# Optimization experiments

Measured on AMD Instinct MI355X. Metric: run time of the kernel, lower is better.

Reference implementation:

```python
import jax, jax.numpy as jnp
import numpy as np
from jax import lax

B, CIN, H, W = 32, 1, 128, 128
SC, CC = 128, 128          # simple / complex channels
C = SC + CC                # 256
KS, STRIDE, PAD = 5, 2, 2  # gabor conv
KDN = 1                    # dn kernel half-size -> 3x3
K_EXC = 25.0
DN = ('NCHW', 'OIHW', 'NCHW')


def _make_gaussian_bank(key):
    k1, k2, k3, k4 = jax.random.split(key, 4)
    thetaD = jnp.abs(jax.random.normal(k1, (C, C)))
    p = jnp.abs(jax.random.normal(k2, (C, C)))
    sig = jnp.abs(jax.random.normal(k3, (C, C)))
    a = jnp.abs(jax.random.normal(k4, (C, C)))
    lin = jnp.linspace(-KDN, KDN, 2 * KDN + 1)
    xv, yv = jnp.meshgrid(lin, lin, indexing='ij')  # torch.meshgrid default 'ij'
    ct = jnp.cos(thetaD)[..., None, None]
    st = jnp.sin(thetaD)[..., None, None]
    xrot = xv * ct + yv * st                        # (C, C, 3, 3)
    yrot = -xv * st + yv * ct
    amp = (a / (2.0 * jnp.pi * p * sig))[..., None, None]
    p2 = (p ** 2)[..., None, None]
    s2 = (sig ** 2)[..., None, None]
    return amp * jnp.exp(-0.5 * (xrot ** 2 / p2 + yrot ** 2 / s2))


def setup_inputs() -> dict:
    key = jax.random.key(0)
    kx, k0, k1, kg = jax.random.split(key, 4)
    x = jax.random.normal(kx, (B, CIN, H, W), dtype=jnp.float32)
    w_q0 = 0.1 * jax.random.normal(k0, (C, CIN, KS, KS), dtype=jnp.float32)
    w_q1 = 0.1 * jax.random.normal(k1, (C, CIN, KS, KS), dtype=jnp.float32)
    gaussian_bank = _make_gaussian_bank(kg).astype(jnp.float32)
    return {"x": x, "w_q0": w_q0, "w_q1": w_q1, "gaussian_bank": gaussian_bank}


def reference(x, w_q0, w_q1, gaussian_bank):
    # Gabor filter bank: two quadrature convs, stride 2, pad 2
    q0 = lax.conv_general_dilated(x, w_q0, (STRIDE, STRIDE),
                                  [(PAD, PAD), (PAD, PAD)], dimension_numbers=DN)
    q1 = lax.conv_general_dilated(x, w_q1, (STRIDE, STRIDE),
                                  [(PAD, PAD), (PAD, PAD)], dimension_numbers=DN)
    s = jax.nn.relu(q0[:, :SC])                                  # simple cells
    c = jnp.sqrt(q0[:, SC:] ** 2 + q1[:, SC:] ** 2) / jnp.sqrt(2.0).astype(x.dtype)
    y = K_EXC * jnp.concatenate((s, c), axis=1)                  # (B, C, 64, 64)
    y = jax.nn.relu(y)                                           # noise_mode=None -> just relu
    # Divisive normalization: gaussian-weighted cross-channel pooling, then divide
    under = lax.conv_general_dilated(y, gaussian_bank, (1, 1),
                                     [(KDN, KDN), (KDN, KDN)], dimension_numbers=DN)
    return y / under
```

## Files before the change

kernel.cpp:

```cpp
#include <hip/hip_runtime.h>
#include <cstddef>


#define NSC 128
#define GSCALE 64.0f

typedef float f4v __attribute__((ext_vector_type(4)));
typedef _Float16 h8v __attribute__((ext_vector_type(8)));

__device__ __forceinline__ short f2h(float f) {
    return __builtin_bit_cast(short, (_Float16)f);
}
__device__ __forceinline__ float h2f(short s) {
    return (float)__builtin_bit_cast(_Float16, s);
}

__global__ __launch_bounds__(256) void prep_g(const float* __restrict__ g,
                                              const float* __restrict__ wq0,
                                              const float* __restrict__ wq1,
                                              short* __restrict__ gf,
                                              float* __restrict__ wt0,
                                              float* __restrict__ wt1) {
    int t = blockIdx.x * 256 + threadIdx.x;
    if (t < 6400) {
        wt0[(t % 25) * 256 + t / 25] = wq0[t];
        wt1[(t % 25) * 256 + t / 25] = wq1[t];
    }
    int co = t & 255, ci = (t >> 8) & 255, kxy = t >> 16;
    float v = g[((size_t)co * 256 + ci) * 9 + kxy] * (1.0f / GSCALE);
    v = fminf(v, 65504.f);
    int wv = co >> 6, m = (co >> 4) & 3, i = co & 15;
    int cc = ci >> 5, q = (ci >> 3) & 3, j = ci & 7;
    int l = q * 16 + i;
    size_t base = ((((size_t)(kxy * 4 + wv) * 4 + m) * 8 + cc)) * 512 + (size_t)l * 8 + j;
    gf[base] = f2h(v);
}

__global__ __launch_bounds__(256) void gabor(const float* __restrict__ x,
                                             const float* __restrict__ wt0,
                                             const float* __restrict__ wt1,
                                             short* __restrict__ y2) {
    __shared__ float xbuf[5][132];
    int oh = blockIdx.x, b = blockIdx.y, c = threadIdx.x;
    for (int i = c; i < 5 * 132; i += 256) (&xbuf[0][0])[i] = 0.f;
    __syncthreads();
    int ihb = oh * 2 - 2;
    for (int i = c; i < 5 * 128; i += 256) {
        int r = i >> 7, col = i & 127;
        int ih = ihb + r;
        if ((unsigned)ih < 128u)
            xbuf[r][col + 2] = x[((size_t)b * 128 + ih) * 128 + col];
    }
    short* yb = y2 + ((size_t)(b * 64 + oh) * 64) * 256 + c;

    if (c < NSC) {
        float w0[25];
#pragma unroll
        for (int i = 0; i < 25; ++i) w0[i] = wt0[i * 256 + c];
        __syncthreads();
        for (int og = 0; og < 16; ++og) {
            int cb = og * 8;
            float q0[4] = {0.f, 0.f, 0.f, 0.f};
#pragma unroll
            for (int ky = 0; ky < 5; ++ky) {
                float xr[12];
                *(float4*)&xr[0] = *(const float4*)&xbuf[ky][cb];
                *(float4*)&xr[4] = *(const float4*)&xbuf[ky][cb + 4];
                *(float4*)&xr[8] = *(const float4*)&xbuf[ky][cb + 8];
#pragma unroll
                for (int j = 0; j < 4; ++j)
#pragma unroll
                    for (int kx = 0; kx < 5; ++kx)
                        q0[j] = fmaf(w0[ky * 5 + kx], xr[2 * j + kx], q0[j]);
            }
#pragma unroll
            for (int j = 0; j < 4; ++j) {
                float v = 25.f * fmaxf(q0[j], 0.f);
                yb[(size_t)(og * 4 + j) * 256] = f2h(v);
            }
        }
    } else {
        float w0[25], w1[25];
#pragma unroll
        for (int i = 0; i < 25; ++i) w0[i] = wt0[i * 256 + c];
#pragma unroll
        for (int i = 0; i < 25; ++i) w1[i] = wt1[i * 256 + c];
        __syncthreads();
        for (int og = 0; og < 16; ++og) {
            int cb = og * 8;
            float q0[4] = {0.f, 0.f, 0.f, 0.f}, q1[4] = {0.f, 0.f, 0.f, 0.f};
#pragma unroll
            for (int ky = 0; ky < 5; ++ky) {
                float xr[12];
                *(float4*)&xr[0] = *(const float4*)&xbuf[ky][cb];
                *(float4*)&xr[4] = *(const float4*)&xbuf[ky][cb + 4];
                *(float4*)&xr[8] = *(const float4*)&xbuf[ky][cb + 8];
#pragma unroll
                for (int j = 0; j < 4; ++j)
#pragma unroll
                    for (int kx = 0; kx < 5; ++kx) {
                        q0[j] = fmaf(w0[ky * 5 + kx], xr[2 * j + kx], q0[j]);
                        q1[j] = fmaf(w1[ky * 5 + kx], xr[2 * j + kx], q1[j]);
                    }
            }
#pragma unroll
            for (int j = 0; j < 4; ++j) {
                float v = 25.f * sqrtf(fmaf(q0[j], q0[j], q1[j] * q1[j])) * 0.70710678118654752f;
                yb[(size_t)(og * 4 + j) * 256] = f2h(v);
            }
        }
    }
}

__device__ __forceinline__ void stage_load(const short* __restrict__ y2, float4* sr,
                                           int b, int r, int half, int tid) {
    if ((unsigned)r < 64u) {
        const short* rowbase = y2 + (size_t)((b * 64 + r) * 64) * 256;
#pragma unroll
        for (int p4 = 0; p4 < 4; ++p4) {
            int i = p4 * 256 + tid;
            int w66 = (i >> 4) + 1, g = i & 15;
            int sg = ((w66 - 1) << 5) + half * 16 + (g ^ (w66 & 7));
            sr[p4] = *(const float4*)(rowbase + (size_t)sg * 8);
        }
    } else {
#pragma unroll
        for (int p4 = 0; p4 < 4; ++p4) sr[p4] = (float4){0.f, 0.f, 0.f, 0.f};
    }
}

__device__ __forceinline__ void stage_write(short* __restrict__ buf, const float4* sr,
                                            int tid) {
#pragma unroll
    for (int p4 = 0; p4 < 4; ++p4) {
        int i = p4 * 256 + tid;
        *(float4*)(buf + (size_t)(16 + i) * 8) = sr[p4];
    }
}

__global__ __launch_bounds__(256, 2) void dn(const short* __restrict__ y2,
                                             const short* __restrict__ gf,
                                             float* __restrict__ out) {
    __shared__ short bbuf[3][66 * 16 * 8];
    int h = blockIdx.x * 2, b = blockIdx.y;
    int tid = threadIdx.x;
    int wv = tid >> 6, l = tid & 63;
    int li = l & 15, lq = l >> 4;

    if (tid < 96) {
        int bi = tid >> 5, t2 = tid & 31;
        int row = (t2 >> 4) ? 65 : 0, g = t2 & 15;
        *(float4*)&bbuf[bi][(row * 16 + g) * 8] = (float4){0.f, 0.f, 0.f, 0.f};
    }

    f4v acc[2][4][4];
#pragma unroll
    for (int hs = 0; hs < 2; ++hs)
#pragma unroll
        for (int m = 0; m < 4; ++m)
#pragma unroll
            for (int n = 0; n < 4; ++n)
                acc[hs][m][n] = (f4v){0.f, 0.f, 0.f, 0.f};

    const h8v* GA = (const h8v*)gf;

    for (int half = 0; half < 2; ++half) {
        float4 sr[4];
        stage_load(y2, sr, b, h - 1, half, tid);
        stage_write(bbuf[(h + 2) % 3], sr, tid);
        stage_load(y2, sr, b, h, half, tid);
        stage_write(bbuf[h % 3], sr, tid);
        __syncthreads();

        for (int ky = 0; ky < 3; ++ky) {
            if (ky < 2)
                stage_load(y2, sr, b, h + ky + 1, half, tid);

            const h8v* B0 = (const h8v*)bbuf[(h + ky + 2) % 3];
            const h8v* B1 = (const h8v*)bbuf[(h + ky) % 3];

            for (int kx = 0; kx < 3; ++kx) {
                int kxy = ky * 3 + kx;
#pragma unroll
                for (int cc = 0; cc < 4; ++cc) {
                    int ccg = half * 4 + cc;
                    h8v Ah[4];
#pragma unroll
                    for (int m = 0; m < 4; ++m) {
                        size_t ab = ((((size_t)(kxy * 4 + wv) * 4 + m) * 8 + ccg)) * 64 + l;
                        Ah[m] = GA[ab];
                    }
#pragma unroll
                    for (int hs = 0; hs < 2; ++hs) {
                        const h8v* BH = hs ? B1 : B0;
                        h8v Bh[4];
#pragma unroll
                        for (int nt = 0; nt < 4; ++nt) {
                            int w66 = nt * 16 + li + kx;
                            int g = (cc * 4 + lq) ^ (w66 & 7);
                            Bh[nt] = BH[w66 * 16 + g];
                        }
#pragma unroll
                        for (int m = 0; m < 4; ++m)
#pragma unroll
                            for (int nt = 0; nt < 4; ++nt)
                                acc[hs][m][nt] = __builtin_amdgcn_mfma_f32_16x16x32_f16(Ah[m], Bh[nt], acc[hs][m][nt], 0, 0, 0);
                    }
                }
            }

            if (ky < 2)
                stage_write(bbuf[(h + ky + 1) % 3], sr, tid);
            __syncthreads();
        }
    }

#pragma unroll
    for (int hs = 0; hs < 2; ++hs) {
        const short* nrow = y2 + (size_t)((b * 64 + h + hs) * 64) * 256;
#pragma unroll
        for (int m = 0; m < 4; ++m) {
            int co = wv * 64 + m * 16 + lq * 4;
#pragma unroll
            for (int nt = 0; nt < 4; ++nt) {
                int w = nt * 16 + li;
                ushort4 nh = *(const ushort4*)(nrow + (size_t)w * 256 + co);
                size_t ob = ((size_t)(b * 256 + co) * 64 + (h + hs)) * 64 + w;
                out[ob]            = h2f((short)nh.x) / (GSCALE * acc[hs][m][nt][0]);
                out[ob + 4096]     = h2f((short)nh.y) / (GSCALE * acc[hs][m][nt][1]);
                out[ob + 2 * 4096] = h2f((short)nh.z) / (GSCALE * acc[hs][m][nt][2]);
                out[ob + 3 * 4096] = h2f((short)nh.w) / (GSCALE * acc[hs][m][nt][3]);
            }
        }
    }
}

extern "C" void kernel_launch(void* const* d_in, const int* in_sizes, int n_in,
                              void* d_out, int out_size, void* d_ws, size_t ws_size,
                              hipStream_t stream) {
    const float* x   = (const float*)d_in[0];
    const float* wq0 = (const float*)d_in[1];
    const float* wq1 = (const float*)d_in[2];
    const float* g   = (const float*)d_in[3];
    float* out = (float*)d_out;
    short* y2 = (short*)d_ws;
    short* gf = y2 + 33554432;
    float* wt0 = (float*)(gf + 589824);
    float* wt1 = wt0 + 6400;

    prep_g<<<2304, 256, 0, stream>>>(g, wq0, wq1, gf, wt0, wt1);
    gabor<<<dim3(64, 32), 256, 0, stream>>>(x, wt0, wt1, y2);
    dn<<<dim3(32, 32), 256, 0, stream>>>(y2, gf, out);
}
```

Baseline: 305.6 us.

## Compute one output row per dn block to raise occupancy

The divisive-normalization kernel now computes one output row per block instead of two. It uses a two-row shared-memory ring instead of three, halves the accumulator registers, doubles the grid and raises launch bounds to four blocks per CU. The aim is more occupancy and more blocks for latency hiding. In exchange, each gaussian-bank A fragment loaded from global memory is reused for one row instead of two, which doubles A-operand traffic.

Result: slower. 513.2 us (+67.9%).

```diff
diff --git a/kernel.cpp b/kernel.cpp
--- a/kernel.cpp
+++ b/kernel.cpp
@@ -138,46 +138,42 @@
     }
 }
 
-__global__ __launch_bounds__(256, 2) void dn(const short* __restrict__ y2,
+__global__ __launch_bounds__(256, 4) void dn(const short* __restrict__ y2,
                                              const short* __restrict__ gf,
                                              float* __restrict__ out) {
-    __shared__ short bbuf[3][66 * 16 * 8];
-    int h = blockIdx.x * 2, b = blockIdx.y;
+    __shared__ short bbuf[2][66 * 16 * 8];
+    int h = blockIdx.x, b = blockIdx.y;
     int tid = threadIdx.x;
     int wv = tid >> 6, l = tid & 63;
     int li = l & 15, lq = l >> 4;
 
-    if (tid < 96) {
-        int bi = tid >> 5, t2 = tid & 31;
-        int row = (t2 >> 4) ? 65 : 0, g = t2 & 15;
+    if (tid < 64) {
+        int bi = tid >> 5;
+        int row = (tid >> 4) & 1 ? 65 : 0, g = tid & 15;
         *(float4*)&bbuf[bi][(row * 16 + g) * 8] = (float4){0.f, 0.f, 0.f, 0.f};
     }
 
-    f4v acc[2][4][4];
-#pragma unroll
-    for (int hs = 0; hs < 2; ++hs)
-#pragma unroll
-        for (int m = 0; m < 4; ++m)
-#pragma unroll
-            for (int n = 0; n < 4; ++n)
-                acc[hs][m][n] = (f4v){0.f, 0.f, 0.f, 0.f};
+    f4v acc[4][4];
+#pragma unroll
+    for (int m = 0; m < 4; ++m)
+#pragma unroll
+        for (int n = 0; n < 4; ++n)
+            acc[m][n] = (f4v){0.f, 0.f, 0.f, 0.f};
 
     const h8v* GA = (const h8v*)gf;
 
     for (int half = 0; half < 2; ++half) {
         float4 sr[4];
         stage_load(y2, sr, b, h - 1, half, tid);
-        stage_write(bbuf[(h + 2) % 3], sr, tid);
-        stage_load(y2, sr, b, h, half, tid);
-        stage_write(bbuf[h % 3], sr, tid);
+        stage_write(bbuf[(h + 1) & 1], sr, tid);
         __syncthreads();
 
         for (int ky = 0; ky < 3; ++ky) {
+            int r = h + ky - 1;
             if (ky < 2)
-                stage_load(y2, sr, b, h + ky + 1, half, tid);
-
-            const h8v* B0 = (const h8v*)bbuf[(h + ky + 2) % 3];
-            const h8v* B1 = (const h8v*)bbuf[(h + ky) % 3];
+                stage_load(y2, sr, b, r + 1, half, tid);
+
+            const h8v* BH = (const h8v*)bbuf[r & 1];
 
             for (int kx = 0; kx < 3; ++kx) {
                 int kxy = ky * 3 + kx;
@@ -190,47 +186,40 @@
                         size_t ab = ((((size_t)(kxy * 4 + wv) * 4 + m) * 8 + ccg)) * 64 + l;
                         Ah[m] = GA[ab];
                     }
-#pragma unroll
-                    for (int hs = 0; hs < 2; ++hs) {
-                        const h8v* BH = hs ? B1 : B0;
-                        h8v Bh[4];
-#pragma unroll
-                        for (int nt = 0; nt < 4; ++nt) {
-                            int w66 = nt * 16 + li + kx;
-                            int g = (cc * 4 + lq) ^ (w66 & 7);
-                            Bh[nt] = BH[w66 * 16 + g];
-                        }
-#pragma unroll
-                        for (int m = 0; m < 4; ++m)
-#pragma unroll
-                            for (int nt = 0; nt < 4; ++nt)
-                                acc[hs][m][nt] = __builtin_amdgcn_mfma_f32_16x16x32_f16(Ah[m], Bh[nt], acc[hs][m][nt], 0, 0, 0);
+                    h8v Bh[4];
+#pragma unroll
+                    for (int nt = 0; nt < 4; ++nt) {
+                        int w66 = nt * 16 + li + kx;
+                        int g = (cc * 4 + lq) ^ (w66 & 7);
+                        Bh[nt] = BH[w66 * 16 + g];
                     }
+#pragma unroll
+                    for (int m = 0; m < 4; ++m)
+#pragma unroll
+                        for (int nt = 0; nt < 4; ++nt)
+                            acc[m][nt] = __builtin_amdgcn_mfma_f32_16x16x32_f16(Ah[m], Bh[nt], acc[m][nt], 0, 0, 0);
                 }
             }
 
             if (ky < 2)
-                stage_write(bbuf[(h + ky + 1) % 3], sr, tid);
+                stage_write(bbuf[(r + 1) & 1], sr, tid);
             __syncthreads();
         }
     }
 
-#pragma unroll
-    for (int hs = 0; hs < 2; ++hs) {
-        const short* nrow = y2 + (size_t)((b * 64 + h + hs) * 64) * 256;
-#pragma unroll
-        for (int m = 0; m < 4; ++m) {
-            int co = wv * 64 + m * 16 + lq * 4;
-#pragma unroll
-            for (int nt = 0; nt < 4; ++nt) {
-                int w = nt * 16 + li;
-                ushort4 nh = *(const ushort4*)(nrow + (size_t)w * 256 + co);
-                size_t ob = ((size_t)(b * 256 + co) * 64 + (h + hs)) * 64 + w;
-                out[ob]            = h2f((short)nh.x) / (GSCALE * acc[hs][m][nt][0]);
-                out[ob + 4096]     = h2f((short)nh.y) / (GSCALE * acc[hs][m][nt][1]);
-                out[ob + 2 * 4096] = h2f((short)nh.z) / (GSCALE * acc[hs][m][nt][2]);
-                out[ob + 3 * 4096] = h2f((short)nh.w) / (GSCALE * acc[hs][m][nt][3]);
-            }
+    const short* nrow = y2 + (size_t)((b * 64 + h) * 64) * 256;
+#pragma unroll
+    for (int m = 0; m < 4; ++m) {
+        int co = wv * 64 + m * 16 + lq * 4;
+#pragma unroll
+        for (int nt = 0; nt < 4; ++nt) {
+            int w = nt * 16 + li;
+            ushort4 nh = *(const ushort4*)(nrow + (size_t)w * 256 + co);
+            size_t ob = ((size_t)(b * 256 + co) * 64 + h) * 64 + w;
+            out[ob]            = h2f((short)nh.x) / (GSCALE * acc[m][nt][0]);
+            out[ob + 4096]     = h2f((short)nh.y) / (GSCALE * acc[m][nt][1]);
+            out[ob + 2 * 4096] = h2f((short)nh.z) / (GSCALE * acc[m][nt][2]);
+            out[ob + 3 * 4096] = h2f((short)nh.w) / (GSCALE * acc[m][nt][3]);
         }
     }
 }
@@ -250,5 +239,5 @@
 
     prep_g<<<2304, 256, 0, stream>>>(g, wq0, wq1, gf, wt0, wt1);
     gabor<<<dim3(64, 32), 256, 0, stream>>>(x, wt0, wt1, y2);
-    dn<<<dim3(32, 32), 256, 0, stream>>>(y2, gf, out);
-}
+    dn<<<dim3(64, 32), 256, 0, stream>>>(y2, gf, out);
+}
```
